# Optimization experiments

Hardware: AMD Instinct MI355X
Metric: run time of the kernel (lower is better)

## Reference

```python
import jax, jax.numpy as jnp
import numpy as np

HID, STEM, BN_OUT, STEM_OUT, MLP = 256, 64, 128, 64, 128
BN_WS, STEM_WS = 5, 17
N, H_BN, W_BN, H_VIS, W_VIS = 4096, 128, 128, 1024, 1024


def setup_inputs() -> dict:
    key = jax.random.key(0)
    ks = jax.random.split(key, 24)
    f32 = jnp.float32
    def rn(k, shape, s=0.05):
        return jax.random.normal(k, shape, f32) * s
    return dict(
        bottleneck=rn(ks[0], (1, HID, H_BN, W_BN), 1.0),
        vis_stem_features=rn(ks[1], (1, STEM, H_VIS, W_VIS), 1.0),
        source_positions_vis=jax.random.uniform(ks[2], (N, 2), f32, 10.0, W_VIS - 10.0),
        pixel_to_sky=rn(ks[3], (N, 2, 2), 0.1),
        fused_h=H_BN, fused_w=W_BN, vis_h=H_VIS, vis_w=W_VIS,
        dw_w=rn(ks[4], (HID, 1, 7, 7)), dw_b=rn(ks[5], (HID,)),
        ln_g=jnp.ones((HID,), f32), ln_b=jnp.zeros((HID,), f32),
        pw1_w=rn(ks[6], (4 * HID, HID)), pw1_b=rn(ks[7], (4 * HID,)),
        pw2_w=rn(ks[8], (HID, 4 * HID)), pw2_b=rn(ks[9], (HID,)),
        cn_gamma=jnp.full((HID,), 1e-2, f32),
        bn1x1_w=rn(ks[10], (BN_OUT, HID, 1, 1)), bn1x1_b=rn(ks[11], (BN_OUT,)),
        st1_w=rn(ks[12], (STEM_OUT, STEM, 3, 3)), st1_b=rn(ks[13], (STEM_OUT,)),
        st2_w=rn(ks[14], (STEM_OUT, STEM_OUT, 3, 3)), st2_b=rn(ks[15], (STEM_OUT,)),
        h1_w=rn(ks[16], (MLP, BN_OUT + STEM_OUT)), h1_b=rn(ks[17], (MLP,)),
        h2_w=rn(ks[18], (MLP, MLP)), h2_b=rn(ks[19], (MLP,)),
        h3_w=rn(ks[20], (3, MLP)),
        h3_b=jnp.array([0.0, 0.0, float(np.log(0.05))], f32),
    )


def _gelu(x):
    return jax.nn.gelu(x, approximate=False)


def _conv2d(x, w, b, padding, groups=1):
    y = jax.lax.conv_general_dilated(
        x, w, (1, 1), [(padding, padding), (padding, padding)],
        dimension_numbers=('NCHW', 'OIHW', 'NCHW'), feature_group_count=groups)
    return y + b[None, :, None, None]


def _bilinear_windows(fm, pos, ws):
    """fm [1,C,H,W], pos [N,2] pixel coords -> [N,C,ws,ws].
    Matches torch grid_sample(mode=bilinear, padding=zeros, align_corners=True)
    with the module's normalize/unnormalize, i.e. direct pixel-coord sampling."""
    C, H, W = fm.shape[1:]
    fm2 = fm[0]
    half = ws // 2
    off = jnp.arange(-half, half + 1, dtype=pos.dtype)
    gy, gx = jnp.meshgrid(off, off, indexing='ij')
    xs = gx[None] + pos[:, 0, None, None]   # [N,ws,ws]
    ys = gy[None] + pos[:, 1, None, None]
    x0 = jnp.floor(xs); y0 = jnp.floor(ys)
    wx1 = xs - x0; wy1 = ys - y0
    x0i = x0.astype(jnp.int32); y0i = y0.astype(jnp.int32)
    def gather(yi, xi, w):
        valid = (yi >= 0) & (yi < H) & (xi >= 0) & (xi < W)
        v = fm2[:, jnp.clip(yi, 0, H - 1), jnp.clip(xi, 0, W - 1)]  # [C,N,ws,ws]
        return v * (w * valid)[None]
    out = (gather(y0i, x0i, (1 - wy1) * (1 - wx1))
           + gather(y0i, x0i + 1, (1 - wy1) * wx1)
           + gather(y0i + 1, x0i, wy1 * (1 - wx1))
           + gather(y0i + 1, x0i + 1, wy1 * wx1))
    return jnp.transpose(out, (1, 0, 2, 3))


def _gauss(ws):
    t = jnp.linspace(-1.0, 1.0, ws)
    yy, xx = jnp.meshgrid(t, t, indexing='ij')
    g = jnp.exp(-(xx ** 2 + yy ** 2) / (2 * 0.4 ** 2))
    return g / g.sum()


def _convnext(x, dw_w, dw_b, ln_g, ln_b, pw1_w, pw1_b, pw2_w, pw2_b, gamma):
    r = x
    x = _conv2d(x, dw_w, dw_b, padding=3, groups=x.shape[1])  # depthwise 7x7
    mu = x.mean(1, keepdims=True)
    var = ((x - mu) ** 2).mean(1, keepdims=True)
    x = (x - mu) / jnp.sqrt(var + 1e-6)
    x = x * ln_g[None, :, None, None] + ln_b[None, :, None, None]
    x = jnp.einsum('nchw,oc->nohw', x, pw1_w) + pw1_b[None, :, None, None]
    x = _gelu(x)
    x = jnp.einsum('nchw,oc->nohw', x, pw2_w) + pw2_b[None, :, None, None]
    return r + gamma[None, :, None, None] * x


def _forward(bottleneck, vis_stem_features, source_positions_vis, pixel_to_sky,
             dw_w, dw_b, ln_g, ln_b, pw1_w, pw1_b, pw2_w, pw2_b, cn_gamma,
             bn1x1_w, bn1x1_b, st1_w, st1_b, st2_w, st2_b,
             h1_w, h1_b, h2_w, h2_b, h3_w, h3_b,
             fused_h, fused_w, vis_h, vis_w):
    scale = jnp.array([fused_w / vis_w, fused_h / vis_h], source_positions_vis.dtype)
    pos_bn = source_positions_vis * scale
    # bottleneck branch: 5x5 windows -> ConvNeXt -> 1x1 conv -> GELU -> gauss pool
    bn_win = _bilinear_windows(bottleneck, pos_bn, BN_WS)              # [N,256,5,5]
    bn_feat = _convnext(bn_win, dw_w, dw_b, ln_g, ln_b, pw1_w, pw1_b, pw2_w, pw2_b, cn_gamma)
    bn_feat = _gelu(_conv2d(bn_feat, bn1x1_w, bn1x1_b, padding=0))     # [N,128,5,5]
    bn_vec = (bn_feat * _gauss(BN_WS)[None, None]).sum((-2, -1))       # [N,128]
    st_win = _bilinear_windows(vis_stem_features, source_positions_vis, STEM_WS)
    st = _gelu(_conv2d(st_win, st1_w, st1_b, padding=1))
    st = _gelu(_conv2d(st, st2_w, st2_b, padding=1))                   # [N,64,17,17]
    st_vec = (st * _gauss(STEM_WS)[None, None]).sum((-2, -1))          # [N,64]
    # head MLP
    x = jnp.concatenate([bn_vec, st_vec], axis=1)                      # [N,192]
    x = _gelu(x @ h1_w.T + h1_b)
    x = _gelu(x @ h2_w.T + h2_b)
    out = x @ h3_w.T + h3_b                                            # [N,3]
    dx_px, dy_px = out[:, 0], out[:, 1]
    log_sigma = jnp.clip(out[:, 2], -6.0, 3.0)
    pix = jnp.stack([dx_px, dy_px], axis=1)                            # [N,2]
    pred_sky = jnp.einsum('nij,nj->ni', pixel_to_sky, pix)             # [N,2]
    confidence = 1.0 / jnp.maximum(jnp.exp(log_sigma), 1e-4)
    return pred_sky, dx_px, dy_px, log_sigma, confidence


def reference(bottleneck, vis_stem_features, source_positions_vis, pixel_to_sky,
              fused_h, fused_w, vis_h, vis_w,
              dw_w, dw_b, ln_g, ln_b, pw1_w, pw1_b, pw2_w, pw2_b, cn_gamma,
              bn1x1_w, bn1x1_b, st1_w, st1_b, st2_w, st2_b,
              h1_w, h1_b, h2_w, h2_b, h3_w, h3_b):
    return _forward(bottleneck, vis_stem_features, source_positions_vis, pixel_to_sky,
                    dw_w, dw_b, ln_g, ln_b, pw1_w, pw1_b, pw2_w, pw2_b, cn_gamma,
                    bn1x1_w, bn1x1_b, st1_w, st1_b, st2_w, st2_b,
                    h1_w, h1_b, h2_w, h2_b, h3_w, h3_b,
                    fused_h, fused_w, vis_h, vis_w)
```

## Files before the change

kernel.cpp:

```cpp
#include <hip/hip_runtime.h>
#include <hip/hip_bf16.h>

#define XSTR 28

typedef short short8 __attribute__((ext_vector_type(8)));
typedef float f32x4  __attribute__((ext_vector_type(4)));

__device__ __forceinline__ float gelu_f(float x){
    return 0.5f*x*(1.0f + erff(x*0.70710678118654752f));
}
__device__ __forceinline__ float gelu_q(float x){
    return x / (1.0f + __expf(-1.702f*x));
}
__device__ __forceinline__ unsigned short f2bf(float f){
    unsigned int u = __float_as_uint(f);
    u += 0x7fffu + ((u>>16)&1u);
    return (unsigned short)(u>>16);
}
__device__ __forceinline__ unsigned int pack2(float a, float b){
    return (unsigned int)f2bf(a) | ((unsigned int)f2bf(b)<<16);
}
__device__ __forceinline__ float bf_lo(unsigned int u){ return __uint_as_float(u<<16); }
__device__ __forceinline__ float bf_hi(unsigned int u){ return __uint_as_float(u & 0xffff0000u); }
__device__ __forceinline__ float bfu(unsigned short v){ return __uint_as_float(((unsigned int)v)<<16); }

__device__ __forceinline__ void fma_row25(const float* __restrict__ row, float w, float* __restrict__ acc){
    const float4* r4 = (const float4*)row;
    float4 a0=r4[0], a1=r4[1], a2=r4[2], a3=r4[3], a4=r4[4], a5=r4[5];
    float a6 = row[24];
    acc[0]+=a0.x*w;  acc[1]+=a0.y*w;  acc[2]+=a0.z*w;  acc[3]+=a0.w*w;
    acc[4]+=a1.x*w;  acc[5]+=a1.y*w;  acc[6]+=a1.z*w;  acc[7]+=a1.w*w;
    acc[8]+=a2.x*w;  acc[9]+=a2.y*w;  acc[10]+=a2.z*w; acc[11]+=a2.w*w;
    acc[12]+=a3.x*w; acc[13]+=a3.y*w; acc[14]+=a3.z*w; acc[15]+=a3.w*w;
    acc[16]+=a4.x*w; acc[17]+=a4.y*w; acc[18]+=a4.z*w; acc[19]+=a4.w*w;
    acc[20]+=a5.x*w; acc[21]+=a5.y*w; acc[22]+=a5.z*w; acc[23]+=a5.w*w;
    acc[24]+=a6*w;
}

__global__ __launch_bounds__(512,4) void bn_branch_mfma(
    const float* __restrict__ bottleneck, const float* __restrict__ pos,
    const float* __restrict__ dw_w, const float* __restrict__ dw_b,
    const float* __restrict__ ln_g, const float* __restrict__ ln_b,
    const float* __restrict__ pw1_b, const float* __restrict__ pw2_b,
    const float* __restrict__ cn_gamma, const float* __restrict__ bn1x1_b,
    const short8* __restrict__ P1v, const short8* __restrict__ P2v,
    const short8* __restrict__ Pbv,
    float* __restrict__ vec_out)
{
    __shared__ __align__(16) unsigned char Xb[64*512];
    __shared__ __align__(16) unsigned char Hc[64*256];
    __shared__ float redA[400], redB[400], muS[56], rsS[56];

    const int n0 = blockIdx.x*2, t = threadIdx.x;
    const int lane = t & 63, w = t >> 6;
    const int mcol = lane & 15, h4 = lane >> 4;
    const int sP = t >> 8, cP = t & 255;

    unsigned int wvp[13];
    float xdw[25];
    {
        const int n = n0 + sP;
        const float px = pos[2*n]*0.125f, py = pos[2*n+1]*0.125f;
        const float fpx = floorf(px), fpy = floorf(py);
        const int ix0 = (int)fpx - 2, iy0 = (int)fpy - 2;
        const float fx = px - fpx, fy = py - fpy;
        const float w00=(1.f-fy)*(1.f-fx), w01=(1.f-fy)*fx, w10=fy*(1.f-fx), w11=fy*fx;
        float wv[25];
        {
            const float* fm = bottleneck + cP*16384;
            float P[6][6];
            #pragma unroll
            for (int r=0;r<6;r++){
                const int y = iy0+r;
                const bool yok = (y>=0)&&(y<128);
                const int yc = y<0?0:(y>127?127:y);
                #pragma unroll
                for (int s=0;s<6;s++){
                    const int x = ix0+s;
                    const bool ok = yok && (x>=0) && (x<128);
                    const int xc = x<0?0:(x>127?127:x);
                    P[r][s] = ok ? fm[yc*128+xc] : 0.f;
                }
            }
            #pragma unroll
            for (int a=0;a<5;a++)
            #pragma unroll
            for (int b=0;b<5;b++)
                wv[a*5+b] = w00*P[a][b]+w01*P[a][b+1]+w10*P[a+1][b]+w11*P[a+1][b+1];
        }
        #pragma unroll
        for (int i=0;i<12;i++) wvp[i] = pack2(wv[2*i], wv[2*i+1]);
        wvp[12] = pack2(wv[24], 0.f);
        {
            float wcr[49];
            const float* wc = dw_w + cP*49;
            #pragma unroll
            for (int k=0;k<49;k++) wcr[k]=wc[k];
            const float bb = dw_b[cP];
            #pragma unroll
            for (int i=0;i<5;i++){
                #pragma unroll
                for (int j=0;j<5;j++){
                    float a = bb;
                    #pragma unroll
                    for (int u=0;u<7;u++){
                        const int y = i+u-3;
                        if (y<0||y>4) continue;
                        #pragma unroll
                        for (int v=0;v<7;v++){
                            const int x = j+v-3;
                            if (x<0||x>4) continue;
                            a += wv[y*5+x]*wcr[u*7+v];
                        }
                    }
                    xdw[i*5+j] = a;
                }
            }
        }
        #pragma unroll
        for (int p=0;p<25;p++){
            const int row = sP*32 + p;
            *(unsigned short*)(Xb + row*512 + ((2*cP) ^ ((row&7)<<4))) = f2bf(xdw[p]);
        }
    }
    __syncthreads();
    if (t < 400){
        const int sp = t>>3, part = t&7;
        const int row = (sp/25)*32 + (sp - (sp/25)*25);
        float a=0.f, b=0.f;
        for (int c=part; c<256; c+=8){
            const float v = bfu(*(const unsigned short*)(Xb + row*512 + ((2*c) ^ ((row&7)<<4))));
            a += v; b += v*v;
        }
        redA[t]=a; redB[t]=b;
    }
    __syncthreads();
    if (t < 50){
        float a=0.f, b=0.f;
        #pragma unroll
        for (int s=0;s<8;s++){ a+=redA[t*8+s]; b+=redB[t*8+s]; }
        const float m = a*(1.f/256.f);
        const float var = b*(1.f/256.f) - m*m;
        muS[t]=m; rsS[t]=rsqrtf(var+1e-6f);
    }
    __syncthreads();
    {
        const float g = ln_g[cP], bb = ln_b[cP];
        #pragma unroll
        for (int p=0;p<25;p++){
            const int row = sP*32 + p;
            const float v = (xdw[p]-muS[sP*25+p])*rsS[sP*25+p]*g + bb;
            *(unsigned short*)(Xb + row*512 + ((2*cP) ^ ((row&7)<<4))) = f2bf(v);
        }
    }
    __syncthreads();

    f32x4 acc2[2][4];
    #pragma unroll
    for (int ml=0;ml<2;ml++)
        #pragma unroll
        for (int nt=0;nt<4;nt++) acc2[ml][nt]=0.f;

    for (int ch=0; ch<8; ++ch){
        const int mt = ch*8 + w;
        f32x4 a1[4];
        #pragma unroll
        for (int nt=0;nt<4;nt++) a1[nt]=0.f;
        #pragma unroll
        for (int kk=0; kk<8; ++kk){
            const short8 av = P1v[((mt<<3)+kk)*64 + lane];
            #pragma unroll
            for (int nt=0; nt<4; ++nt){
                const int row = nt*16 + mcol;
                const int ad = row*512 + ((kk*64 + h4*16) ^ ((row&7)<<4));
                const short8 bv = *(const short8*)(Xb + ad);
                a1[nt] = __builtin_amdgcn_mfma_f32_16x16x32_bf16(av, bv, a1[nt], 0,0,0);
            }
        }
        {
            const float4 b1v = *(const float4*)(pw1_b + mt*16 + h4*4);
            #pragma unroll
            for (int nt=0; nt<4; ++nt){
                const int row = nt*16 + mcol;
                const float g0 = gelu_q(a1[nt].x + b1v.x);
                const float g1 = gelu_q(a1[nt].y + b1v.y);
                const float g2 = gelu_q(a1[nt].z + b1v.z);
                const float g3 = gelu_q(a1[nt].w + b1v.w);
                const int ad = row*256 + ((w*32 + h4*8) ^ ((row&7)<<4));
                *(uint2*)(Hc + ad) = make_uint2(pack2(g0,g1), pack2(g2,g3));
            }
        }
        __syncthreads();
        #pragma unroll
        for (int ml=0; ml<2; ++ml){
            const int mtc = w*2 + ml;
            #pragma unroll
            for (int kk2=0; kk2<4; ++kk2){
                const short8 av = P2v[(mtc*32 + (ch*4 + kk2))*64 + lane];
                #pragma unroll
                for (int nt=0; nt<4; ++nt){
                    const int row = nt*16 + mcol;
                    const int ad = row*256 + ((kk2*64 + h4*16) ^ ((row&7)<<4));
                    const short8 bv = *(const short8*)(Hc + ad);
                    acc2[ml][nt] = __builtin_amdgcn_mfma_f32_16x16x32_bf16(av, bv, acc2[ml][nt], 0,0,0);
                }
            }
        }
        __syncthreads();
    }

    #pragma unroll
    for (int ml=0; ml<2; ++ml){
        const int c0 = (w*2+ml)*16 + h4*4;
        const float4 gm = *(const float4*)(cn_gamma + c0);
        const float4 b2 = *(const float4*)(pw2_b + c0);
        #pragma unroll
        for (int nt=0; nt<4; ++nt){
            const int row = nt*16 + mcol;
            const int ad = row*512 + ((2*c0) ^ ((row&7)<<4));
            const float f0 = gm.x*(acc2[ml][nt].x + b2.x);
            const float f1 = gm.y*(acc2[ml][nt].y + b2.y);
            const float f2 = gm.z*(acc2[ml][nt].z + b2.z);
            const float f3 = gm.w*(acc2[ml][nt].w + b2.w);
            *(uint2*)(Xb + ad) = make_uint2(pack2(f0,f1), pack2(f2,f3));
        }
    }
    __syncthreads();
    #pragma unroll
    for (int p=0;p<25;p++){
        const int row = sP*32 + p;
        unsigned short* ptr = (unsigned short*)(Xb + row*512 + ((2*cP) ^ ((row&7)<<4)));
        const float r = (p&1) ? bf_hi(wvp[p>>1]) : bf_lo(wvp[p>>1]);
        *ptr = f2bf(bfu(*ptr) + r);
    }
    __syncthreads();

    {
        f32x4 a3[4];
        #pragma unroll
        for (int nt=0;nt<4;nt++) a3[nt]=0.f;
        #pragma unroll
        for (int kk=0; kk<8; ++kk){
            const short8 av = Pbv[((w<<3)+kk)*64 + lane];
            #pragma unroll
            for (int nt=0; nt<4; ++nt){
                const int row = nt*16 + mcol;
                const int ad = row*512 + ((kk*64 + h4*16) ^ ((row&7)<<4));
                const short8 bv = *(const short8*)(Xb + ad);
                a3[nt] = __builtin_amdgcn_mfma_f32_16x16x32_bf16(av, bv, a3[nt], 0,0,0);
            }
        }
        const float4 bb = *(const float4*)(bn1x1_b + w*16 + h4*4);
        float e5[5];
        #pragma unroll
        for (int a=0;a<5;a++){
            const float ta = -1.f + 0.5f*a;
            e5[a] = expf(-3.125f*ta*ta);
        }
        const float Sv = e5[0]+e5[1]+e5[2]+e5[3]+e5[4];
        const float invS = 1.0f/(Sv*Sv);
        float sA[2][4];
        #pragma unroll
        for (int s=0;s<2;s++)
            #pragma unroll
            for (int j=0;j<4;j++) sA[s][j]=0.f;
        #pragma unroll
        for (int nt=0; nt<4; ++nt){
            const int row = nt*16 + mcol;
            const int s = row>>5, p = row&31;
            if (p < 25){
                const int pa = p/5, pb = p - pa*5;
                const float g = e5[pa]*e5[pb];
                sA[s][0] += g*gelu_q(a3[nt].x + bb.x);
                sA[s][1] += g*gelu_q(a3[nt].y + bb.y);
                sA[s][2] += g*gelu_q(a3[nt].z + bb.z);
                sA[s][3] += g*gelu_q(a3[nt].w + bb.w);
            }
        }
        #pragma unroll
        for (int off=1; off<16; off<<=1){
            #pragma unroll
            for (int s=0;s<2;s++)
                #pragma unroll
                for (int j=0;j<4;j++) sA[s][j] += __shfl_xor(sA[s][j], off);
        }
        if (mcol == 0){
            const int o = w*16 + h4*4;
            #pragma unroll
            for (int s=0;s<2;s++){
                float* vo = vec_out + (n0+s)*192 + o;
                vo[0]=sA[s][0]*invS; vo[1]=sA[s][1]*invS;
                vo[2]=sA[s][2]*invS; vo[3]=sA[s][3]*invS;
            }
        }
    }
}

__global__ __launch_bounds__(256) void prepack_bn_kernel(
    const float* __restrict__ W1, const float* __restrict__ W2, const float* __restrict__ Wb,
    unsigned short* __restrict__ P1, unsigned short* __restrict__ P2, unsigned short* __restrict__ Pb)
{
    const int tid = blockIdx.x*256 + threadIdx.x;
    const float* src; unsigned short* dst; int row, col, stride, idx;
    if (tid < 32768){
        idx = tid;
        const int frag = idx>>6, l = idx&63;
        row = (frag>>3)*16 + (l&15); col = (frag&7)*32 + (l>>4)*8; stride = 256;
        src = W1; dst = P1;
    } else if (tid < 65536){
        idx = tid - 32768;
        const int frag = idx>>6, l = idx&63;
        row = (frag>>5)*16 + (l&15); col = (frag&31)*32 + (l>>4)*8; stride = 1024;
        src = W2; dst = P2;
    } else if (tid < 69632){
        idx = tid - 65536;
        const int frag = idx>>6, l = idx&63;
        row = (frag>>3)*16 + (l&15); col = (frag&7)*32 + (l>>4)*8; stride = 256;
        src = Wb; dst = Pb;
    } else return;
    const float* s = src + row*stride + col;
    unsigned int v[4];
    #pragma unroll
    for (int j=0;j<4;j++) v[j] = pack2(s[2*j], s[2*j+1]);
    *(uint4*)(dst + (size_t)idx*8) = make_uint4(v[0],v[1],v[2],v[3]);
}

__global__ __launch_bounds__(256,2) void bn_branch_valu(
    const float* __restrict__ bottleneck, const float* __restrict__ pos,
    const float* __restrict__ dw_w, const float* __restrict__ dw_b,
    const float* __restrict__ ln_g, const float* __restrict__ ln_b,
    const float* __restrict__ pw1_w, const float* __restrict__ pw1_b,
    const float* __restrict__ pw2_w, const float* __restrict__ pw2_b,
    const float* __restrict__ cn_gamma,
    const float* __restrict__ bn1x1_w, const float* __restrict__ bn1x1_b,
    float* __restrict__ vec_out)
{
    __shared__ float xln[256*XSTR];
    __shared__ float hbuf[256*XSTR];
    __shared__ float redA[200], redB[200];
    __shared__ float mu[25], rs[25];

    const int n = blockIdx.x;
    const int t = threadIdx.x;
    const int c = t;

    const float px = pos[2*n]*0.125f, py = pos[2*n+1]*0.125f;
    const float fpx = floorf(px), fpy = floorf(py);
    const int ix0 = (int)fpx - 2, iy0 = (int)fpy - 2;
    const float fx = px - fpx, fy = py - fpy;
    const float w00=(1.f-fy)*(1.f-fx), w01=(1.f-fy)*fx, w10=fy*(1.f-fx), w11=fy*fx;

    float wv[25];
    {
        const float* fm = bottleneck + c*16384;
        float P[6][6];
        #pragma unroll
        for (int r=0;r<6;r++){
            const int y = iy0+r;
            const bool yok = (y>=0)&&(y<128);
            const int yc = y<0?0:(y>127?127:y);
            #pragma unroll
            for (int s=0;s<6;s++){
                const int x = ix0+s;
                const bool ok = yok && (x>=0) && (x<128);
                const int xc = x<0?0:(x>127?127:x);
                P[r][s] = ok ? fm[yc*128+xc] : 0.f;
            }
        }
        #pragma unroll
        for (int a=0;a<5;a++)
        #pragma unroll
        for (int b=0;b<5;b++)
            wv[a*5+b] = w00*P[a][b]+w01*P[a][b+1]+w10*P[a+1][b]+w11*P[a+1][b+1];
    }
    {
        float wcr[49];
        const float* wc = dw_w + c*49;
        #pragma unroll
        for (int k=0;k<49;k++) wcr[k]=wc[k];
        const float bb = dw_b[c];
        #pragma unroll
        for (int i=0;i<5;i++){
            #pragma unroll
            for (int j=0;j<5;j++){
                float a = bb;
                #pragma unroll
                for (int u=0;u<7;u++){
                    const int y = i+u-3;
                    if (y<0||y>4) continue;
                    #pragma unroll
                    for (int v=0;v<7;v++){
                        const int x = j+v-3;
                        if (x<0||x>4) continue;
                        a += wv[y*5+x]*wcr[u*7+v];
                    }
                }
                xln[c*XSTR + i*5+j] = a;
            }
        }
    }
    __syncthreads();
    if (t < 200){
        const int p = t>>3, s = t&7;
        float a=0.f, b=0.f;
        for (int cc=s; cc<256; cc+=8){
            const float v = xln[cc*XSTR+p];
            a += v; b += v*v;
        }
        redA[t]=a; redB[t]=b;
    }
    __syncthreads();
    if (t < 25){
        float a=0.f, b=0.f;
        #pragma unroll
        for (int s=0;s<8;s++){ a+=redA[t*8+s]; b+=redB[t*8+s]; }
        const float m = a*(1.f/256.f);
        const float var = b*(1.f/256.f) - m*m;
        mu[t]=m; rs[t]=rsqrtf(var+1e-6f);
    }
    __syncthreads();
    {
        const float g = ln_g[c], bb = ln_b[c];
        #pragma unroll
        for (int p=0;p<25;p++)
            xln[c*XSTR+p] = (xln[c*XSTR+p]-mu[p])*rs[p]*g + bb;
    }
    __syncthreads();
    float acc2[25];
    #pragma unroll
    for (int p=0;p<25;p++) acc2[p]=0.f;
    for (int r=0;r<4;r++){
        const int o = r*256 + t;
        float h[25];
        {
            const float b1 = pw1_b[o];
            #pragma unroll
            for (int p=0;p<25;p++) h[p]=b1;
            const float* wr = pw1_w + o*256;
            for (int cc=0;cc<256;cc++)
                fma_row25(xln + cc*XSTR, wr[cc], h);
            #pragma unroll
            for (int p=0;p<25;p++) h[p]=gelu_f(h[p]);
        }
        __syncthreads();
        #pragma unroll
        for (int p=0;p<25;p++) hbuf[t*XSTR+p]=h[p];
        __syncthreads();
        {
            const float* w2 = pw2_w + t*1024 + r*256;
            for (int k=0;k<256;k++)
                fma_row25(hbuf + k*XSTR, w2[k], acc2);
        }
    }
    {
        const float gam = cn_gamma[c], b2 = pw2_b[c];
        #pragma unroll
        for (int p=0;p<25;p++)
            xln[c*XSTR+p] = wv[p] + gam*(acc2[p]+b2);
    }
    __syncthreads();
    if (t < 128){
        float acc[25];
        #pragma unroll
        for (int p=0;p<25;p++) acc[p]=0.f;
        const float* wr = bn1x1_w + t*256;
        for (int cc=0;cc<256;cc++)
            fma_row25(xln + cc*XSTR, wr[cc], acc);
        const float b = bn1x1_b[t];
        float e5[5];
        #pragma unroll
        for (int a=0;a<5;a++){
            const float ta = -1.f + 0.5f*a;
            e5[a] = expf(-3.125f*ta*ta);
        }
        const float Sv = e5[0]+e5[1]+e5[2]+e5[3]+e5[4];
        float res = 0.f;
        #pragma unroll
        for (int a=0;a<5;a++){
            float rowa = 0.f;
            #pragma unroll
            for (int bb=0;bb<5;bb++)
                rowa += e5[bb]*gelu_f(acc[a*5+bb]+b);
            res += e5[a]*rowa;
        }
        vec_out[n*192+t] = res/(Sv*Sv);
    }
}

__global__ __launch_bounds__(256) void prepack_kernel(
    const float* __restrict__ W1, const float* __restrict__ W2,
    unsigned short* __restrict__ Ap)
{
    const int tid = blockIdx.x*256 + threadIdx.x;
    if (tid >= 9216) return;
    int r = tid;
    const int conv = r / 4608; r -= conv*4608;
    const int k = r / 512;     r -= k*512;
    const int s = r / 256;     r -= s*256;
    const int w = r / 64;
    const int l = r - w*64;
    const float* W = conv ? W2 : W1;
    const int o  = w*16 + (l & 15);
    const int c0 = s*32 + (l >> 4)*8;
    unsigned int v[4];
    #pragma unroll
    for (int jj=0; jj<4; jj++){
        const float f0 = W[o*576 + (c0+2*jj  )*9 + k];
        const float f1 = W[o*576 + (c0+2*jj+1)*9 + k];
        v[jj] = pack2(f0, f1);
    }
    uint4* dst = (uint4*)(Ap + (size_t)tid*8);
    *dst = make_uint4(v[0], v[1], v[2], v[3]);
}

#define STEM_CONV(SRC, AP, ACC)                                                     \
    for (int k=0;k<9;k++){                                                          \
        const int dy = k/3 - 1, dx = (k - (k/3)*3) - 1;                             \
        for (int s=0;s<2;s++){                                                      \
            const short8 av = (AP)[k*512 + s*256 + w*64 + lane];                    \
            const int cb = s*64 + h*16;                                             \
            _Pragma("unroll")                                                       \
            for (int nt=0; nt<19; nt++){                                            \
                const int p  = nt*16 + m;                                           \
                const int py = (p*241)>>12;                                         \
                const int px = p - py*17;                                           \
                const int y = py + dy, x = px + dx;                                 \
                const bool ok = ((unsigned)y < 17u) && ((unsigned)x < 17u);         \
                const int pp = ok ? (y*17 + x) : 305;                               \
                const int ad = pp*128 + (cb ^ ((pp&7)<<4));                         \
                const short8 bv = *(const short8*)((SRC) + ad);                     \
                ACC[nt] = __builtin_amdgcn_mfma_f32_16x16x32_bf16(av, bv, ACC[nt], 0, 0, 0); \
            }                                                                       \
        }                                                                           \
    }

__global__ __launch_bounds__(256,2) void stem_branch_kernel(
    const float* __restrict__ vis,
    const float* __restrict__ pos,
    const short8* __restrict__ Ap1,
    const float* __restrict__ st1_b,
    const float* __restrict__ st2_b,
    float* __restrict__ vec_out)
{
    __shared__ __align__(16) unsigned char sXt[306*128];
    __shared__ __align__(16) unsigned char sC1[306*128];
    __shared__ float redS[64];

    const int n = blockIdx.x;
    const int t = threadIdx.x;
    const int lane = t & 63;
    const int m = t & 15;
    const int h = (t >> 4) & 3;
    const int w = t >> 6;

    const float fpx0 = pos[2*n], fpy0 = pos[2*n+1];
    const float fpx = floorf(fpx0), fpy = floorf(fpy0);
    const int ix0 = (int)fpx - 8, iy0 = (int)fpy - 8;
    const float fx = fpx0-fpx, fy = fpy0-fpy;
    const float w00=(1.f-fy)*(1.f-fx), w01=(1.f-fy)*fx, w10=fy*(1.f-fx), w11=fy*fx;

    if (t < 32)      *(unsigned int*)(sXt + 305*128 + t*4) = 0u;
    else if (t < 64) *(unsigned int*)(sC1 + 305*128 + (t-32)*4) = 0u;

    for (int task = t; task < 64*17; task += 256){
        const int c  = task & 63;
        const int py = task >> 6;
        const float* r0 = vis + c*1048576 + (iy0+py)*1024 + ix0;
        float a[18], b[18];
        #pragma unroll
        for (int kk=0; kk<18; kk++){ a[kk]=r0[kk]; b[kk]=r0[1024+kk]; }
        #pragma unroll
        for (int px=0; px<17; px++){
            const float v = w00*a[px] + w01*a[px+1] + w10*b[px] + w11*b[px+1];
            const int p = py*17 + px;
            *(unsigned short*)(sXt + p*128 + ((2*c) ^ ((p&7)<<4))) = f2bf(v);
        }
    }
    __syncthreads();

    f32x4 acc[19];
    #pragma unroll
    for (int nt=0; nt<19; nt++) acc[nt] = 0.f;
    STEM_CONV(sXt, Ap1, acc)

    {
        const int obase = w*16 + h*4;
        const float bo0 = st1_b[obase], bo1 = st1_b[obase+1];
        const float bo2 = st1_b[obase+2], bo3 = st1_b[obase+3];
        #pragma unroll
        for (int nt=0; nt<19; nt++){
            const int p = nt*16 + m;
            if (p < 304){
                const unsigned r01 = pack2(gelu_f(acc[nt].x+bo0), gelu_f(acc[nt].y+bo1));
                const unsigned r23 = pack2(gelu_f(acc[nt].z+bo2), gelu_f(acc[nt].w+bo3));
                const int ad = p*128 + ((2*obase) ^ ((p&7)<<4));
                *(uint2*)(sC1 + ad) = make_uint2(r01, r23);
            }
        }
    }
    __syncthreads();

    const short8* Ap2 = Ap1 + 4608;
    #pragma unroll
    for (int nt=0; nt<19; nt++) acc[nt] = 0.f;
    STEM_CONV(sC1, Ap2, acc)

    {
        const int obase = w*16 + h*4;
        const float bo0 = st2_b[obase], bo1 = st2_b[obase+1];
        const float bo2 = st2_b[obase+2], bo3 = st2_b[obase+3];
        float s0=0.f, s1=0.f, s2=0.f, s3=0.f;
        #pragma unroll
        for (int nt=0; nt<19; nt++){
            const int p = nt*16 + m;
            if (p < 289){
                const int py = (p*241)>>12;
                const int px = p - py*17;
                const float ty = -1.f + 0.125f*py;
                const float tx = -1.f + 0.125f*px;
                const float g = expf(-3.125f*(ty*ty + tx*tx));
                s0 += g*gelu_f(acc[nt].x+bo0);
                s1 += g*gelu_f(acc[nt].y+bo1);
                s2 += g*gelu_f(acc[nt].z+bo2);
                s3 += g*gelu_f(acc[nt].w+bo3);
            }
        }
        #pragma unroll
        for (int off=1; off<16; off<<=1){
            s0 += __shfl_xor(s0, off);
            s1 += __shfl_xor(s1, off);
            s2 += __shfl_xor(s2, off);
            s3 += __shfl_xor(s3, off);
        }
        if (m == 0){
            redS[obase]   = s0;
            redS[obase+1] = s1;
            redS[obase+2] = s2;
            redS[obase+3] = s3;
        }
    }
    __syncthreads();
    if (t < 64){
        float Sv = 0.f;
        #pragma unroll
        for (int j=0;j<17;j++){
            const float tj = -1.f + 0.125f*j;
            Sv += expf(-3.125f*tj*tj);
        }
        vec_out[n*192+128+t] = redS[t] / (Sv*Sv);
    }
}

__global__ __launch_bounds__(128) void head16_kernel(
    const float* __restrict__ vec, const float* __restrict__ p2s,
    const float* __restrict__ h1_w, const float* __restrict__ h1_b,
    const float* __restrict__ h2_w, const float* __restrict__ h2_b,
    const float* __restrict__ h3_w, const float* __restrict__ h3_b,
    float* __restrict__ out, int N)
{
    __shared__ float v[16][192];
    __shared__ float x1s[16][132];
    __shared__ float x2s[16][132];
    __shared__ float o3s[16][4];
    const int n0 = blockIdx.x*16, t = threadIdx.x;

    for (int idx=t; idx<16*192; idx+=128){
        const int s = idx/192, k = idx - s*192;
        v[s][k] = vec[n0*192 + idx];
    }
    __syncthreads();
    {
        const int o = t;
        float acc[16];
        const float b = h1_b[o];
        #pragma unroll
        for (int s=0;s<16;s++) acc[s]=b;
        const float4* wr = (const float4*)(h1_w + o*192);
        for (int k4=0;k4<48;k4++){
            const float4 wv4 = wr[k4];
            #pragma unroll
            for (int s=0;s<16;s++){
                const float4 vv = *(const float4*)&v[s][k4*4];
                acc[s] += wv4.x*vv.x + wv4.y*vv.y + wv4.z*vv.z + wv4.w*vv.w;
            }
        }
        #pragma unroll
        for (int s=0;s<16;s++) x1s[s][o] = gelu_f(acc[s]);
    }
    __syncthreads();
    {
        const int o = t;
        float acc[16];
        const float b = h2_b[o];
        #pragma unroll
        for (int s=0;s<16;s++) acc[s]=b;
        const float4* wr = (const float4*)(h2_w + o*128);
        for (int k4=0;k4<32;k4++){
            const float4 wv4 = wr[k4];
            #pragma unroll
            for (int s=0;s<16;s++){
                const float4 vv = *(const float4*)&x1s[s][k4*4];
                acc[s] += wv4.x*vv.x + wv4.y*vv.y + wv4.z*vv.z + wv4.w*vv.w;
            }
        }
        #pragma unroll
        for (int s=0;s<16;s++) x2s[s][o] = gelu_f(acc[s]);
    }
    __syncthreads();
    if (t < 48){
        const int j = t>>4, s = t&15;
        float a = h3_b[j];
        const float* wr = h3_w + j*128;
        for (int k=0;k<128;k++) a += x2s[s][k]*wr[k];
        o3s[s][j] = a;
    }
    __syncthreads();
    if (t < 16){
        const int s = t, n = n0 + s;
        const float dx = o3s[s][0], dy = o3s[s][1];
        float ls = o3s[s][2];
        ls = ls < -6.f ? -6.f : (ls > 3.f ? 3.f : ls);
        const float s0 = p2s[n*4+0]*dx + p2s[n*4+1]*dy;
        const float s1 = p2s[n*4+2]*dx + p2s[n*4+3]*dy;
        const float conf = 1.0f/fmaxf(expf(ls), 1e-4f);
        out[2*n]   = s0;
        out[2*n+1] = s1;
        out[2*N+n] = dx;
        out[3*N+n] = dy;
        out[4*N+n] = ls;
        out[5*N+n] = conf;
    }
}

extern "C" void kernel_launch(void* const* d_in, const int* in_sizes, int n_in,
                              void* d_out, int out_size, void* d_ws, size_t ws_size,
                              hipStream_t stream)
{
    (void)n_in; (void)out_size;
    const float* bottleneck = (const float*)d_in[0];
    const float* vis        = (const float*)d_in[1];
    const float* pos        = (const float*)d_in[2];
    const float* p2s        = (const float*)d_in[3];
    const float* dw_w  = (const float*)d_in[8];
    const float* dw_b  = (const float*)d_in[9];
    const float* ln_g  = (const float*)d_in[10];
    const float* ln_b  = (const float*)d_in[11];
    const float* pw1_w = (const float*)d_in[12];
    const float* pw1_b = (const float*)d_in[13];
    const float* pw2_w = (const float*)d_in[14];
    const float* pw2_b = (const float*)d_in[15];
    const float* gam   = (const float*)d_in[16];
    const float* b1w   = (const float*)d_in[17];
    const float* b1b   = (const float*)d_in[18];
    const float* s1w   = (const float*)d_in[19];
    const float* s1b   = (const float*)d_in[20];
    const float* s2w   = (const float*)d_in[21];
    const float* s2b   = (const float*)d_in[22];
    const float* h1w   = (const float*)d_in[23];
    const float* h1b   = (const float*)d_in[24];
    const float* h2w   = (const float*)d_in[25];
    const float* h2b   = (const float*)d_in[26];
    const float* h3w   = (const float*)d_in[27];
    const float* h3b   = (const float*)d_in[28];

    const int N = in_sizes[2]/2;
    float* vec = (float*)d_ws;
    const size_t vec_bytes = (size_t)N*192*sizeof(float);
    unsigned short* Apack = (unsigned short*)((char*)d_ws + vec_bytes);
    unsigned short* P1 = Apack + 73728;
    unsigned short* P2 = P1 + 262144;
    unsigned short* Pb = P2 + 262144;
    const size_t need = vec_bytes + 147456u + (262144u+262144u+32768u)*2u;

    hipMemsetAsync(d_ws, 0, vec_bytes, stream);

    prepack_kernel<<<36, 256, 0, stream>>>(s1w, s2w, Apack);

    if (ws_size >= need){
        prepack_bn_kernel<<<272, 256, 0, stream>>>(pw1_w, pw2_w, b1w, P1, P2, Pb);
        bn_branch_mfma<<<N/2, 512, 0, stream>>>(bottleneck, pos, dw_w, dw_b, ln_g, ln_b,
                                                pw1_b, pw2_b, gam, b1b,
                                                (const short8*)P1, (const short8*)P2, (const short8*)Pb,
                                                vec);
    } else {
        bn_branch_valu<<<N, 256, 0, stream>>>(bottleneck, pos, dw_w, dw_b, ln_g, ln_b,
                                              pw1_w, pw1_b, pw2_w, pw2_b, gam, b1w, b1b, vec);
    }
    stem_branch_kernel<<<N, 256, 0, stream>>>(vis, pos, (const short8*)Apack, s1b, s2b, vec);
    head16_kernel<<<N/16, 128, 0, stream>>>(vec, p2s, h1w, h1b, h2w, h2b, h3w, h3b,
                                            (float*)d_out, N);
}
```

Measured before the change: 907.4 us.

## Precompute stem-conv LDS address table and use tanh-approx GELU in stem

Replaces the per-MFMA computation of neighbor pixel indices, bounds checks and swizzle in the stem 3x3 convs with a shared-memory lookup table built once per block. The two channel halves are now fetched with an XOR on the table address. LDS buffers shrink to 290 rows. The exact erf GELU in both stem epilogues is swapped for a sigmoid form of the tanh approximation, and gelu_q itself changes from the 1.702x sigmoid to that tanh-style formula. This cuts integer address ALU work and transcendental cost, but adds extra LDS reads for the table and a small numerical deviation from exact GELU.

```diff
diff --git a/kernel.cpp b/kernel.cpp
--- a/kernel.cpp
+++ b/kernel.cpp
@@ -10,7 +10,8 @@
     return 0.5f*x*(1.0f + erff(x*0.70710678118654752f));
 }
 __device__ __forceinline__ float gelu_q(float x){
-    return x / (1.0f + __expf(-1.702f*x));
+    const float z = 1.5957691216057308f*x*(1.0f + 0.044715f*x*x);
+    return x / (1.0f + __expf(-z));
 }
 __device__ __forceinline__ unsigned short f2bf(float f){
     unsigned int u = __float_as_uint(f);
@@ -513,24 +514,18 @@
     *dst = make_uint4(v[0], v[1], v[2], v[3]);
 }
 
-#define STEM_CONV(SRC, AP, ACC)                                                     \
+#define STEM_CONV_T(SRC, AP)                                                        \
     for (int k=0;k<9;k++){                                                          \
-        const int dy = k/3 - 1, dx = (k - (k/3)*3) - 1;                             \
-        for (int s=0;s<2;s++){                                                      \
-            const short8 av = (AP)[k*512 + s*256 + w*64 + lane];                    \
-            const int cb = s*64 + h*16;                                             \
-            _Pragma("unroll")                                                       \
-            for (int nt=0; nt<19; nt++){                                            \
-                const int p  = nt*16 + m;                                           \
-                const int py = (p*241)>>12;                                         \
-                const int px = p - py*17;                                           \
-                const int y = py + dy, x = px + dx;                                 \
-                const bool ok = ((unsigned)y < 17u) && ((unsigned)x < 17u);         \
-                const int pp = ok ? (y*17 + x) : 305;                               \
-                const int ad = pp*128 + (cb ^ ((pp&7)<<4));                         \
-                const short8 bv = *(const short8*)((SRC) + ad);                     \
-                ACC[nt] = __builtin_amdgcn_mfma_f32_16x16x32_bf16(av, bv, ACC[nt], 0, 0, 0); \
-            }                                                                       \
+        const short8 a0 = (AP)[k*512       + w*64 + lane];                          \
+        const short8 a1 = (AP)[k*512 + 256 + w*64 + lane];                          \
+        const unsigned short* trow = sTab + m*171 + k;                              \
+        _Pragma("unroll")                                                           \
+        for (int nt=0; nt<19; nt++){                                                \
+            const int ad0 = ((int)trow[nt*9]) ^ h16;                                \
+            const short8 bv0 = *(const short8*)((SRC) + ad0);                       \
+            acc[nt] = __builtin_amdgcn_mfma_f32_16x16x32_bf16(a0, bv0, acc[nt], 0,0,0); \
+            const short8 bv1 = *(const short8*)((SRC) + (ad0 ^ 64));                \
+            acc[nt] = __builtin_amdgcn_mfma_f32_16x16x32_bf16(a1, bv1, acc[nt], 0,0,0); \
         }                                                                           \
     }
 
@@ -542,15 +537,16 @@
     const float* __restrict__ st2_b,
     float* __restrict__ vec_out)
 {
-    __shared__ __align__(16) unsigned char sXt[306*128];
-    __shared__ __align__(16) unsigned char sC1[306*128];
+    __shared__ __align__(16) unsigned char sXt[290*128];
+    __shared__ __align__(16) unsigned char sC1[290*128];
+    __shared__ unsigned short sTab[16*171];
     __shared__ float redS[64];
 
     const int n = blockIdx.x;
     const int t = threadIdx.x;
     const int lane = t & 63;
     const int m = t & 15;
-    const int h = (t >> 4) & 3;
+    const int h16 = ((t >> 4) & 3) * 16;
     const int w = t >> 6;
 
     const float fpx0 = pos[2*n], fpy0 = pos[2*n+1];
@@ -559,8 +555,20 @@
     const float fx = fpx0-fpx, fy = fpy0-fpy;
     const float w00=(1.f-fy)*(1.f-fx), w01=(1.f-fy)*fx, w10=fy*(1.f-fx), w11=fy*fx;
 
-    if (t < 32)      *(unsigned int*)(sXt + 305*128 + t*4) = 0u;
-    else if (t < 64) *(unsigned int*)(sC1 + 305*128 + (t-32)*4) = 0u;
+    if (t < 32)      *(unsigned int*)(sXt + 289*128 + t*4) = 0u;
+    else if (t < 64) *(unsigned int*)(sC1 + 289*128 + (t-32)*4) = 0u;
+
+    for (int idx = t; idx < 16*171; idx += 256){
+        const int mm = idx/171, rem = idx - mm*171;
+        const int nt = rem/9, k = rem - nt*9;
+        const int p = nt*16 + mm;
+        const int py = (p*241)>>12, px = p - py*17;
+        const int dyy = k/3 - 1, dxx = k - (k/3)*3 - 1;
+        const int y = py+dyy, x = px+dxx;
+        const bool ok = ((unsigned)y < 17u) && ((unsigned)x < 17u);
+        const int pp = ok ? (y*17+x) : 289;
+        sTab[idx] = (unsigned short)(pp*128 + ((pp&7)<<4));
+    }
 
     for (int task = t; task < 64*17; task += 256){
         const int c  = task & 63;
@@ -581,18 +589,18 @@
     f32x4 acc[19];
     #pragma unroll
     for (int nt=0; nt<19; nt++) acc[nt] = 0.f;
-    STEM_CONV(sXt, Ap1, acc)
-
-    {
-        const int obase = w*16 + h*4;
+    STEM_CONV_T(sXt, Ap1)
+
+    {
+        const int obase = w*16 + (h16>>2);
         const float bo0 = st1_b[obase], bo1 = st1_b[obase+1];
         const float bo2 = st1_b[obase+2], bo3 = st1_b[obase+3];
         #pragma unroll
         for (int nt=0; nt<19; nt++){
             const int p = nt*16 + m;
-            if (p < 304){
-                const unsigned r01 = pack2(gelu_f(acc[nt].x+bo0), gelu_f(acc[nt].y+bo1));
-                const unsigned r23 = pack2(gelu_f(acc[nt].z+bo2), gelu_f(acc[nt].w+bo3));
+            if (p < 289){
+                const unsigned r01 = pack2(gelu_q(acc[nt].x+bo0), gelu_q(acc[nt].y+bo1));
+                const unsigned r23 = pack2(gelu_q(acc[nt].z+bo2), gelu_q(acc[nt].w+bo3));
                 const int ad = p*128 + ((2*obase) ^ ((p&7)<<4));
                 *(uint2*)(sC1 + ad) = make_uint2(r01, r23);
             }
@@ -603,10 +611,10 @@
     const short8* Ap2 = Ap1 + 4608;
     #pragma unroll
     for (int nt=0; nt<19; nt++) acc[nt] = 0.f;
-    STEM_CONV(sC1, Ap2, acc)
-
-    {
-        const int obase = w*16 + h*4;
+    STEM_CONV_T(sC1, Ap2)
+
+    {
+        const int obase = w*16 + (h16>>2);
         const float bo0 = st2_b[obase], bo1 = st2_b[obase+1];
         const float bo2 = st2_b[obase+2], bo3 = st2_b[obase+3];
         float s0=0.f, s1=0.f, s2=0.f, s3=0.f;
@@ -619,10 +627,10 @@
                 const float ty = -1.f + 0.125f*py;
                 const float tx = -1.f + 0.125f*px;
                 const float g = expf(-3.125f*(ty*ty + tx*tx));
-                s0 += g*gelu_f(acc[nt].x+bo0);
-                s1 += g*gelu_f(acc[nt].y+bo1);
-                s2 += g*gelu_f(acc[nt].z+bo2);
-                s3 += g*gelu_f(acc[nt].w+bo3);
+                s0 += g*gelu_q(acc[nt].x+bo0);
+                s1 += g*gelu_q(acc[nt].y+bo1);
+                s2 += g*gelu_q(acc[nt].z+bo2);
+                s3 += g*gelu_q(acc[nt].w+bo3);
             }
         }
         #pragma unroll
```

Measured after the change: 866.0 us. -4.6%, faster.
